# Kernel tuning notes

Measured on AMD Instinct MI355X. Metric: run time of the kernel, lower is better.

The kernel has to match this reference:

```python
import jax, jax.numpy as jnp
import numpy as np

N_FEATURES = 128
POISSON_LAMBDA = 2.0
B = 500000


def setup_inputs() -> dict:
    key = jax.random.key(0)
    kx, km = jax.random.split(key)
    x = jax.random.normal(kx, (B, N_FEATURES), dtype=jnp.float32)
    mask = (jax.random.uniform(km, (B, N_FEATURES)) > 0.1).astype(jnp.float32)
    return {"x": x, "mask": mask}


def reference(x, mask):
    """Vectorized equivalent of the per-row Python loop:
    per row, draw n ~ Poisson(lambda) clipped to [0, F-1]; if the row has
    >1 valid features, mask n = min(n, n_valid-1) uniformly-random valid
    features (set to 0 in both x and the validity mask).
    Uniform random subset selection is done by ranking random scores:
    valid positions get U(0,1) scores, invalid get -1; the n highest-scoring
    valid positions form a uniform random n-subset of the valid indices.
    """
    Bn, F = x.shape
    kp, ku = jax.random.split(jax.random.key(42))
    valid = mask > 0.5
    n_valid = valid.sum(axis=1)  # (B,) int
    n = jnp.clip(jax.random.poisson(kp, POISSON_LAMBDA, (Bn,)), 0, F - 1)
    n = jnp.where(n_valid > 1, jnp.minimum(n, n_valid - 1), 0)  # (B,)
    scores = jnp.where(valid, jax.random.uniform(ku, (Bn, F)), -1.0)
    order = jnp.argsort(-scores, axis=1)          # columns sorted by descending score
    ranks = jnp.argsort(order, axis=1)            # rank of each column (0 = highest score)
    drop = (ranks < n[:, None]) & valid           # n random valid positions per row
    random_mask = jnp.where(drop, 0.0, 1.0).astype(x.dtype)
    return x * random_mask, mask * random_mask
```

## Files before the change

### kernel.cpp

```cpp
#include <hip/hip_runtime.h>
#include <cstdint>
#include <math.h>


#define DH __host__ __device__ __forceinline__

DH uint32_t rotl32(uint32_t v, uint32_t r) { return (v << r) | (v >> (32u - r)); }

DH void tf2x32(uint32_t k0, uint32_t k1, uint32_t x0, uint32_t x1,
               uint32_t& o0, uint32_t& o1) {
  const uint32_t k2 = k0 ^ k1 ^ 0x1BD11BDAu;
  x0 += k0; x1 += k1;
  x0 += x1; x1 = rotl32(x1, 13); x1 ^= x0;
  x0 += x1; x1 = rotl32(x1, 15); x1 ^= x0;
  x0 += x1; x1 = rotl32(x1, 26); x1 ^= x0;
  x0 += x1; x1 = rotl32(x1,  6); x1 ^= x0;
  x0 += k1; x1 += k2 + 1u;
  x0 += x1; x1 = rotl32(x1, 17); x1 ^= x0;
  x0 += x1; x1 = rotl32(x1, 29); x1 ^= x0;
  x0 += x1; x1 = rotl32(x1, 16); x1 ^= x0;
  x0 += x1; x1 = rotl32(x1, 24); x1 ^= x0;
  x0 += k2; x1 += k0 + 2u;
  x0 += x1; x1 = rotl32(x1, 13); x1 ^= x0;
  x0 += x1; x1 = rotl32(x1, 15); x1 ^= x0;
  x0 += x1; x1 = rotl32(x1, 26); x1 ^= x0;
  x0 += x1; x1 = rotl32(x1,  6); x1 ^= x0;
  x0 += k0; x1 += k1 + 3u;
  x0 += x1; x1 = rotl32(x1, 17); x1 ^= x0;
  x0 += x1; x1 = rotl32(x1, 29); x1 ^= x0;
  x0 += x1; x1 = rotl32(x1, 16); x1 ^= x0;
  x0 += x1; x1 = rotl32(x1, 24); x1 ^= x0;
  x0 += k1; x1 += k2 + 4u;
  x0 += x1; x1 = rotl32(x1, 13); x1 ^= x0;
  x0 += x1; x1 = rotl32(x1, 15); x1 ^= x0;
  x0 += x1; x1 = rotl32(x1, 26); x1 ^= x0;
  x0 += x1; x1 = rotl32(x1,  6); x1 ^= x0;
  x0 += k2; x1 += k0 + 5u;
  o0 = x0; o1 = x1;
}

__device__ __forceinline__ float u01(uint32_t bits) {
  return __uint_as_float((bits >> 9) | 0x3f800000u) - 1.0f;
}

struct PoisKeys { uint32_t s0[24]; uint32_t s1[24]; };

__global__ __launch_bounds__(256) void rfm_kernel(
    const float* __restrict__ x, const float* __restrict__ mask,
    float* __restrict__ out, int B,
    uint32_t ku0, uint32_t ku1, PoisKeys pk) {
  const int tid = (int)threadIdx.x;
  const int row = (int)blockIdx.x * 16 + (tid >> 4);
  if (row >= B) return;
  const int li = tid & 15;
  const int wl = tid & 63;
  const int gb = wl & 48;
  const size_t base = (size_t)row * 128u + (size_t)(li * 8);
  const size_t NF = (size_t)B * 128u;

  const float4 ma = *(const float4*)(mask + base);
  const float4 mb = *(const float4*)(mask + base + 4);
  const float4 xa = *(const float4*)(x + base);
  const float4 xb = *(const float4*)(x + base + 4);

  float lg;
  {
    uint32_t b0, b1;
    tf2x32(pk.s0[li], pk.s1[li], 0u, (uint32_t)row, b0, b1);
    lg = (float)log((double)u01(b0 ^ b1));
  }
  float lp = 0.0f;
  int k = 0;
#pragma unroll
  for (int j = 0; j < 8; ++j) {
    const float lj = __shfl(lg, gb + j);
    k += (lp > -2.0f) ? 1 : 0;
    lp += lj;
  }
  if (lp > -2.0f) {
#pragma unroll
    for (int j = 8; j < 16; ++j) {
      const float lj = __shfl(lg, gb + j);
      k += (lp > -2.0f) ? 1 : 0;
      lp += lj;
    }
    if (lp > -2.0f) {
      uint32_t c0, c1;
      const int i2 = 16 + (li & 7);
      tf2x32(pk.s0[i2], pk.s1[i2], 0u, (uint32_t)row, c0, c1);
      const float lg2 = (float)log((double)u01(c0 ^ c1));
#pragma unroll
      for (int j = 0; j < 8; ++j) {
        const float lj = __shfl(lg2, gb + j);
        k += (lp > -2.0f) ? 1 : 0;
        lp += lj;
      }
    }
  }
  int n = k - 1;

  float mv[8] = {ma.x, ma.y, ma.z, ma.w, mb.x, mb.y, mb.z, mb.w};
  float s[8];
  int nv = 0;
  const uint32_t idx0 = (uint32_t)row * 128u + (uint32_t)(li * 8);
#pragma unroll
  for (int j = 0; j < 8; ++j) {
    uint32_t b0, b1;
    tf2x32(ku0, ku1, 0u, idx0 + (uint32_t)j, b0, b1);
    const bool valid = mv[j] > 0.5f;
    s[j] = valid ? u01(b0 ^ b1) : -1.0f;
    nv += valid ? 1 : 0;
  }
#pragma unroll
  for (int off = 8; off; off >>= 1) nv += __shfl_xor(nv, off);

  n = (nv > 1) ? min(n, nv - 1) : 0;

  uint32_t dropbits = 0u;
  for (int t = 0; t < n; ++t) {
    float bs = s[0];
    int bj = 0;
#pragma unroll
    for (int j = 1; j < 8; ++j) {
      if (s[j] > bs) { bs = s[j]; bj = j; }
    }
    int bc = (li << 3) + bj;
#pragma unroll
    for (int off = 8; off; off >>= 1) {
      const float os = __shfl_xor(bs, off);
      const int   oc = __shfl_xor(bc, off);
      if (os > bs || (os == bs && oc < bc)) { bs = os; bc = oc; }
    }
    const bool own = (bc >> 3) == li;
    const int  lj  = bc & 7;
#pragma unroll
    for (int j = 0; j < 8; ++j) {
      if (own && lj == j) { s[j] = -2.0f; dropbits |= (1u << j); }
    }
  }

  float xv[8] = {xa.x, xa.y, xa.z, xa.w, xb.x, xb.y, xb.z, xb.w};
#pragma unroll
  for (int j = 0; j < 8; ++j) {
    if ((dropbits >> j) & 1u) { xv[j] = 0.0f; mv[j] = 0.0f; }
  }
  {
    float4 o;
    o.x = xv[0]; o.y = xv[1]; o.z = xv[2]; o.w = xv[3];
    *(float4*)(out + base) = o;
    o.x = xv[4]; o.y = xv[5]; o.z = xv[6]; o.w = xv[7];
    *(float4*)(out + base + 4) = o;
    o.x = mv[0]; o.y = mv[1]; o.z = mv[2]; o.w = mv[3];
    *(float4*)(out + NF + base) = o;
    o.x = mv[4]; o.y = mv[5]; o.z = mv[6]; o.w = mv[7];
    *(float4*)(out + NF + base + 4) = o;
  }
}

extern "C" void kernel_launch(void* const* d_in, const int* in_sizes, int n_in,
                              void* d_out, int out_size, void* d_ws, size_t ws_size,
                              hipStream_t stream) {
  const float* x    = (const float*)d_in[0];
  const float* mask = (const float*)d_in[1];
  float* out = (float*)d_out;

  const int B = in_sizes[0] / 128;

  uint32_t kp0, kp1, ku0, ku1;
  tf2x32(0u, 42u, 0u, 0u, kp0, kp1);
  tf2x32(0u, 42u, 0u, 1u, ku0, ku1);

  PoisKeys pk;
  {
    uint32_t r0 = kp0, r1 = kp1;
    for (int it = 0; it < 24; ++it) {
      uint32_t s0, s1, t0, t1;
      tf2x32(r0, r1, 0u, 1u, s0, s1);
      tf2x32(r0, r1, 0u, 0u, t0, t1);
      pk.s0[it] = s0; pk.s1[it] = s1;
      r0 = t0; r1 = t1;
    }
  }

  const int rowsPerBlock = 16;
  const int blocks = (B + rowsPerBlock - 1) / rowsPerBlock;
  rfm_kernel<<<blocks, 256, 0, stream>>>(x, mask, out, B, ku0, ku1, pk);
}
```

Before: 237.1 us.

## Partition rows by Poisson count to skip RNG work for zero-drop rows

Adds a pre-pass kernel that computes each row's Poisson draw once per row and compacts rows into two lists: rows with zero drops and rows needing masking. The main kernel then handles zero-drop rows as pure copies and runs the per-element Threefry scoring and top-n selection only on the others, so divergence within a wavefront goes away. This costs two extra launches, a workspace list, atomics and an indirect row lookup that scatters memory access. The original fused kernel is kept as a fallback when the workspace is too small.

```diff
diff --git a/kernel.cpp b/kernel.cpp
--- a/kernel.cpp
+++ b/kernel.cpp
@@ -43,9 +43,142 @@
   return __uint_as_float((bits >> 9) | 0x3f800000u) - 1.0f;
 }
 
-struct PoisKeys { uint32_t s0[24]; uint32_t s1[24]; };
-
-__global__ __launch_bounds__(256) void rfm_kernel(
+struct PoisKeys { uint32_t s0[32]; uint32_t s1[32]; };
+
+__global__ void zero_ctrs(uint32_t* __restrict__ ctrs) {
+  if (threadIdx.x < 2) ctrs[threadIdx.x] = 0u;
+}
+
+__global__ __launch_bounds__(256) void pois_part_kernel(
+    uint32_t* __restrict__ list, uint32_t* __restrict__ ctrs, int B,
+    PoisKeys pk) {
+  const int row = (int)(blockIdx.x * 256u + threadIdx.x);
+  const bool active = row < B;
+  int n = 0;
+  if (active) {
+    float lp = 0.0f;
+    int k = 0;
+    for (int it = 0; it < 32; ++it) {
+      if (lp <= -2.0f) break;
+      uint32_t b0, b1;
+      tf2x32(pk.s0[it], pk.s1[it], 0u, (uint32_t)row, b0, b1);
+      ++k;
+      lp += (float)log((double)u01(b0 ^ b1));
+    }
+    n = k - 1;
+  }
+  const int lane = (int)(threadIdx.x & 63u);
+  const bool isZ = active && (n == 0);
+  const bool isH = active && (n > 0);
+  const unsigned long long below = lane ? (~0ull >> (64 - lane)) : 0ull;
+  const unsigned long long mz = __ballot(isZ);
+  const unsigned long long mh = __ballot(isH);
+  if (isZ) {
+    const int cnt = __popcll(mz);
+    const int lid = __popcll(mz & below);
+    int basep = 0;
+    if (lid == 0) basep = (int)atomicAdd(&ctrs[0], (uint32_t)cnt);
+    basep = __shfl(basep, (int)(__ffsll((unsigned long long)mz) - 1));
+    list[basep + lid] = (uint32_t)row;
+  }
+  if (isH) {
+    const int cnt = __popcll(mh);
+    const int lid = __popcll(mh & below);
+    int basep = 0;
+    if (lid == 0) basep = (int)atomicAdd(&ctrs[1], (uint32_t)cnt);
+    basep = __shfl(basep, (int)(__ffsll((unsigned long long)mh) - 1));
+    list[(B - 1) - (basep + lid)] = ((uint32_t)row << 5) | (uint32_t)min(n, 31);
+  }
+}
+
+__global__ __launch_bounds__(256) void rfm_main(
+    const float* __restrict__ x, const float* __restrict__ mask,
+    const uint32_t* __restrict__ list, const uint32_t* __restrict__ ctrs,
+    float* __restrict__ out, int B, uint32_t ku0, uint32_t ku1) {
+  const int G = (int)((blockIdx.x * 256u + threadIdx.x) >> 4);
+  if (G >= B) return;
+  const int li = (int)(threadIdx.x & 15u);
+  const int zc = (int)ctrs[0];
+
+  int row, n = 0;
+  bool hashp;
+  if (G < zc) {
+    row = (int)list[G];
+    hashp = false;
+  } else {
+    const uint32_t e = list[(B - 1) - (G - zc)];
+    row = (int)(e >> 5);
+    n = (int)(e & 31u);
+    hashp = true;
+  }
+
+  const size_t base = (size_t)row * 128u + (size_t)(li * 8);
+  const size_t NF = (size_t)B * 128u;
+
+  const float4 ma = *(const float4*)(mask + base);
+  const float4 mb = *(const float4*)(mask + base + 4);
+  const float4 xa = *(const float4*)(x + base);
+  const float4 xb = *(const float4*)(x + base + 4);
+  float mv[8] = {ma.x, ma.y, ma.z, ma.w, mb.x, mb.y, mb.z, mb.w};
+  float xv[8] = {xa.x, xa.y, xa.z, xa.w, xb.x, xb.y, xb.z, xb.w};
+
+  if (hashp) {
+    float s[8];
+    int nv = 0;
+    const uint32_t idx0 = (uint32_t)row * 128u + (uint32_t)(li * 8);
+#pragma unroll
+    for (int j = 0; j < 8; ++j) {
+      uint32_t b0, b1;
+      tf2x32(ku0, ku1, 0u, idx0 + (uint32_t)j, b0, b1);
+      const bool valid = mv[j] > 0.5f;
+      s[j] = valid ? u01(b0 ^ b1) : -1.0f;
+      nv += valid ? 1 : 0;
+    }
+#pragma unroll
+    for (int off = 8; off; off >>= 1) nv += __shfl_xor(nv, off);
+
+    n = (nv > 1) ? min(n, nv - 1) : 0;
+
+    uint32_t dropbits = 0u;
+    for (int t = 0; t < n; ++t) {
+      float bs = s[0];
+      int bj = 0;
+#pragma unroll
+      for (int j = 1; j < 8; ++j) {
+        if (s[j] > bs) { bs = s[j]; bj = j; }
+      }
+      int bc = (li << 3) + bj;
+#pragma unroll
+      for (int off = 8; off; off >>= 1) {
+        const float os = __shfl_xor(bs, off);
+        const int   oc = __shfl_xor(bc, off);
+        if (os > bs || (os == bs && oc < bc)) { bs = os; bc = oc; }
+      }
+      const bool own = (bc >> 3) == li;
+      const int  lj  = bc & 7;
+#pragma unroll
+      for (int j = 0; j < 8; ++j) {
+        if (own && lj == j) { s[j] = -2.0f; dropbits |= (1u << j); }
+      }
+    }
+#pragma unroll
+    for (int j = 0; j < 8; ++j) {
+      if ((dropbits >> j) & 1u) { xv[j] = 0.0f; mv[j] = 0.0f; }
+    }
+  }
+
+  float4 o;
+  o.x = xv[0]; o.y = xv[1]; o.z = xv[2]; o.w = xv[3];
+  *(float4*)(out + base) = o;
+  o.x = xv[4]; o.y = xv[5]; o.z = xv[6]; o.w = xv[7];
+  *(float4*)(out + base + 4) = o;
+  o.x = mv[0]; o.y = mv[1]; o.z = mv[2]; o.w = mv[3];
+  *(float4*)(out + NF + base) = o;
+  o.x = mv[4]; o.y = mv[5]; o.z = mv[6]; o.w = mv[7];
+  *(float4*)(out + NF + base + 4) = o;
+}
+
+__global__ __launch_bounds__(256) void rfm_fused(
     const float* __restrict__ x, const float* __restrict__ mask,
     float* __restrict__ out, int B,
     uint32_t ku0, uint32_t ku1, PoisKeys pk) {
@@ -53,8 +186,7 @@
   const int row = (int)blockIdx.x * 16 + (tid >> 4);
   if (row >= B) return;
   const int li = tid & 15;
-  const int wl = tid & 63;
-  const int gb = wl & 48;
+  const int gb = (tid & 63) & 48;
   const size_t base = (size_t)row * 128u + (size_t)(li * 8);
   const size_t NF = (size_t)B * 128u;
 
@@ -113,7 +245,6 @@
   }
 #pragma unroll
   for (int off = 8; off; off >>= 1) nv += __shfl_xor(nv, off);
-
   n = (nv > 1) ? min(n, nv - 1) : 0;
 
   uint32_t dropbits = 0u;
@@ -144,17 +275,15 @@
   for (int j = 0; j < 8; ++j) {
     if ((dropbits >> j) & 1u) { xv[j] = 0.0f; mv[j] = 0.0f; }
   }
-  {
-    float4 o;
-    o.x = xv[0]; o.y = xv[1]; o.z = xv[2]; o.w = xv[3];
-    *(float4*)(out + base) = o;
-    o.x = xv[4]; o.y = xv[5]; o.z = xv[6]; o.w = xv[7];
-    *(float4*)(out + base + 4) = o;
-    o.x = mv[0]; o.y = mv[1]; o.z = mv[2]; o.w = mv[3];
-    *(float4*)(out + NF + base) = o;
-    o.x = mv[4]; o.y = mv[5]; o.z = mv[6]; o.w = mv[7];
-    *(float4*)(out + NF + base + 4) = o;
-  }
+  float4 o;
+  o.x = xv[0]; o.y = xv[1]; o.z = xv[2]; o.w = xv[3];
+  *(float4*)(out + base) = o;
+  o.x = xv[4]; o.y = xv[5]; o.z = xv[6]; o.w = xv[7];
+  *(float4*)(out + base + 4) = o;
+  o.x = mv[0]; o.y = mv[1]; o.z = mv[2]; o.w = mv[3];
+  *(float4*)(out + NF + base) = o;
+  o.x = mv[4]; o.y = mv[5]; o.z = mv[6]; o.w = mv[7];
+  *(float4*)(out + NF + base + 4) = o;
 }
 
 extern "C" void kernel_launch(void* const* d_in, const int* in_sizes, int n_in,
@@ -173,7 +302,7 @@
   PoisKeys pk;
   {
     uint32_t r0 = kp0, r1 = kp1;
-    for (int it = 0; it < 24; ++it) {
+    for (int it = 0; it < 32; ++it) {
       uint32_t s0, s1, t0, t1;
       tf2x32(r0, r1, 0u, 1u, s0, s1);
       tf2x32(r0, r1, 0u, 0u, t0, t1);
@@ -182,7 +311,16 @@
     }
   }
 
-  const int rowsPerBlock = 16;
-  const int blocks = (B + rowsPerBlock - 1) / rowsPerBlock;
-  rfm_kernel<<<blocks, 256, 0, stream>>>(x, mask, out, B, ku0, ku1, pk);
-}
+  const size_t wsNeeded = (size_t)B * 4u + 8u;
+  if (ws_size < wsNeeded) {
+    rfm_fused<<<(B + 15) / 16, 256, 0, stream>>>(x, mask, out, B, ku0, ku1, pk);
+    return;
+  }
+
+  uint32_t* list = (uint32_t*)d_ws;
+  uint32_t* ctrs = (uint32_t*)((char*)d_ws + (size_t)B * 4u);
+  zero_ctrs<<<1, 64, 0, stream>>>(ctrs);
+  pois_part_kernel<<<(B + 255) / 256, 256, 0, stream>>>(list, ctrs, B, pk);
+  rfm_main<<<(B + 15) / 16, 256, 0, stream>>>(x, mask, list, ctrs, out, B,
+                                              ku0, ku1);
+}
```

Result: slower. 398.0 us (+67.9%).
